# Optimization experiments

Hardware: AMD Instinct MI355X
Metric: run time of the kernel (lower is better)

## Reference

```python
import jax, jax.numpy as jnp
import numpy as np

B, X, C = 8192, 8, 512        # batch, map_num, img_dim==tex_dim
P, Y = 8, 1000                # n_prompts, cls_num
FAKE = 16                     # fake prompt width (hardcoded in module)
F = 2048                      # feat_dim
CLS = 1000                    # cls_num
IN_DIM = P * X * FAKE         # 1024
SF = 64.0


def setup_inputs() -> dict:
    key = jax.random.key(0)
    ks = jax.random.split(key, 8)
    s = 0.02
    return {
        "img_f": jax.random.normal(ks[0], (B, X, C), jnp.float32),
        "tex_f": jax.random.normal(ks[1], (P, Y, C), jnp.float32),
        "fake_cls": jax.random.normal(ks[2], (P, FAKE, C), jnp.float32),
        "fc_w": jax.random.normal(ks[3], (C, C), jnp.float32) * s,
        "fc_b": jnp.zeros((C,), jnp.float32),
        "bn1_g": jnp.ones((IN_DIM,), jnp.float32),
        "bn1_b": jnp.zeros((IN_DIM,), jnp.float32),
        "w1": jax.random.normal(ks[4], (F, IN_DIM), jnp.float32) * s,
        "b1": jnp.zeros((F,), jnp.float32),
        "bn2_g": jnp.ones((F,), jnp.float32),
        "bn2_b": jnp.zeros((F,), jnp.float32),
        "w2": jax.random.normal(ks[5], (CLS, F), jnp.float32) * s,
        "b2": jnp.zeros((CLS,), jnp.float32),
    }


def _bn(x, g, b, eps=1e-5):
    # BatchNorm1d in training mode: batch mean / biased batch var
    m = x.mean(axis=0)
    v = x.var(axis=0)
    return (x - m) * jax.lax.rsqrt(v + eps) * g + b


def reference(img_f, tex_f, fake_cls, fc_w, fc_b, bn1_g, bn1_b, w1, b1,
              bn2_g, bn2_b, w2, b2):
    # independent L2 norm over feature dim, scaled by x_sf=64
    img_n = img_f / (jnp.linalg.norm(img_f, axis=-1, keepdims=True) + 1e-6) * SF
    tex_n = tex_f / (jnp.linalg.norm(tex_f, axis=-1, keepdims=True) + 1e-6) * SF
    # prompt attention over the class axis
    tex_fc = jnp.einsum('pyc,dc->pyd', tex_n, fc_w) + fc_b          # fc(tex_f)
    attn = jax.nn.softmax(jnp.einsum('pxc,pyc->pxy', fake_cls, tex_fc), axis=-1)
    tex_a = jnp.einsum('pxy,pyc->pxc', attn, tex_n)                  # (P,16,C)
    # cross-modal relation: 'b x c, y d c -> b yxd' (icomp/tcomp are Identity)
    cp = jnp.einsum('bxc,pdc->bpxd', img_n, tex_a).reshape(img_n.shape[0], -1)
    # prt_fc: BN -> Linear -> ELU -> BN -> Linear
    h = jax.nn.elu(_bn(cp, bn1_g, bn1_b) @ w1.T + b1)
    return _bn(h, bn2_g, bn2_b) @ w2.T + b2
```

## Files before the change

### kernel.cpp

```cpp
#include <hip/hip_runtime.h>
#include <math.h>


typedef __attribute__((ext_vector_type(8))) short bf16x8;
typedef __attribute__((ext_vector_type(4))) float f32x4;

__device__ __forceinline__ float waveSum(float v) {
#pragma unroll
    for (int o = 32; o > 0; o >>= 1) v += __shfl_xor(v, o);
    return v;
}
__device__ __forceinline__ float waveMax(float v) {
#pragma unroll
    for (int o = 32; o > 0; o >>= 1) v = fmaxf(v, __shfl_xor(v, o));
    return v;
}
__device__ __forceinline__ unsigned short f2bf(float x) {
    union { float f; unsigned u; } v; v.f = x;
    unsigned r = v.u + 0x7FFFu + ((v.u >> 16) & 1u);
    return (unsigned short)(r >> 16);
}
__device__ __forceinline__ float bf2f(unsigned short h) {
    union { unsigned u; float f; } v; v.u = ((unsigned)h) << 16; return v.f;
}
__device__ __forceinline__ void gload16(const void* g, const void* l) {
    __builtin_amdgcn_global_load_lds((const __attribute__((address_space(1))) void*)g,
                                     (__attribute__((address_space(3))) void*)l, 16, 0, 0);
}
__device__ __forceinline__ int xcd_swz(int d, int n) {
    int q = n >> 3;
    return (d & 7) * q + (d >> 3);
}
#define SBAR __builtin_amdgcn_sched_barrier(0)

__global__ __launch_bounds__(256) void k_prep(const float* __restrict__ tex_f,
                                              unsigned short* __restrict__ texn,
                                              const float* __restrict__ fake_cls,
                                              const float* __restrict__ fc_w,
                                              unsigned short* __restrict__ g_bf) {
    __shared__ float sred[4];
    __shared__ float fcls[512];
    int bid = blockIdx.x, t = threadIdx.x;
    if (bid < 8000) {
        const float* r = tex_f + (size_t)bid * 512;
        float2 v = *(const float2*)(r + t * 2);
        float ss = v.x * v.x + v.y * v.y;
        ss = waveSum(ss);
        if ((t & 63) == 0) sred[t >> 6] = ss;
        __syncthreads();
        float tot = sred[0] + sred[1] + sred[2] + sred[3];
        float sc = 64.f / (sqrtf(tot) + 1e-6f);
        unsigned u = (unsigned)f2bf(v.x * sc) | ((unsigned)f2bf(v.y * sc) << 16);
        *(unsigned*)(texn + (size_t)bid * 512 + t * 2) = u;
    } else {
        int row = bid - 8000;
        fcls[t]       = fake_cls[row * 512 + t];
        fcls[t + 256] = fake_cls[row * 512 + t + 256];
        __syncthreads();
        float a0 = 0.f, a1 = 0.f;
        for (int d = 0; d < 512; ++d) {
            float fv = fcls[d];
            a0 = fmaf(fv, fc_w[d * 512 + t], a0);
            a1 = fmaf(fv, fc_w[d * 512 + t + 256], a1);
        }
        g_bf[row * 512 + t]       = f2bf(a0);
        g_bf[row * 512 + t + 256] = f2bf(a1);
    }
}

__global__ __launch_bounds__(256) void k_wsum_sm(const float* __restrict__ logit,
                                                 const unsigned short* __restrict__ texn,
                                                 float* __restrict__ part) {
    int yt = blockIdx.x, p = blockIdx.y, t = threadIdx.x;
    int lane = t & 63, w = t >> 6;
    __shared__ float wl[16][63];
    __shared__ float ms[16], iss[16];
    const int y0 = yt * 63;
    const int ylen = min(63, 1000 - y0);
#pragma unroll
    for (int rr = 0; rr < 4; ++rr) {
        int x = w * 4 + rr;
        const float* lr = logit + ((size_t)p * 16 + x) * 1000;
        float m = -3.0e38f;
        for (int y = lane; y < 1000; y += 64) m = fmaxf(m, lr[y]);
        m = waveMax(m);
        float s = 0.f;
        for (int y = lane; y < 1000; y += 64) s += expf(lr[y] - m);
        s = waveSum(s);
        if (lane == 0) { ms[x] = m; iss[x] = 1.f / s; }
    }
    __syncthreads();
    for (int idx = t; idx < 16 * ylen; idx += 256) {
        int x = idx / ylen, y = idx % ylen;
        wl[x][y] = expf(logit[((size_t)p * 16 + x) * 1000 + y0 + y] - ms[x]) * iss[x];
    }
    __syncthreads();
    int c0 = t * 2;
    const unsigned short* tp = texn + ((size_t)p * 1000 + y0) * 512 + c0;
    float a0[16], a1[16];
#pragma unroll
    for (int x = 0; x < 16; ++x) { a0[x] = 0.f; a1[x] = 0.f; }
    for (int y = 0; y < ylen; ++y) {
        unsigned u = *(const unsigned*)(tp + (size_t)y * 512);
        float lo = bf2f((unsigned short)(u & 0xffff));
        float hi = bf2f((unsigned short)(u >> 16));
#pragma unroll
        for (int x = 0; x < 16; ++x) {
            float ww = wl[x][y];
            a0[x] = fmaf(ww, lo, a0[x]);
            a1[x] = fmaf(ww, hi, a1[x]);
        }
    }
#pragma unroll
    for (int x = 0; x < 16; ++x) {
        float* dst = part + ((size_t)((yt * 8 + p) * 16 + x)) * 512 + c0;
        dst[0] = a0[x];
        dst[1] = a1[x];
    }
}

__global__ __launch_bounds__(256) void k_texa_red(const float* __restrict__ part,
                                                  unsigned short* __restrict__ texa) {
    int row = blockIdx.x, t = threadIdx.x;
    int p = row >> 4, x = row & 15;
    int c = t * 2;
    float s0 = 0.f, s1 = 0.f;
#pragma unroll
    for (int yt = 0; yt < 16; ++yt) {
        const float* src = part + ((size_t)((yt * 8 + p) * 16 + x)) * 512 + c;
        s0 += src[0];
        s1 += src[1];
    }
    unsigned u = (unsigned)f2bf(s0) | ((unsigned)f2bf(s1) << 16);
    *(unsigned*)(texa + (size_t)row * 512 + c) = u;
}

__global__ __launch_bounds__(256) void k_colstat_bf(const unsigned short* __restrict__ src,
                                                    float* __restrict__ ps,
                                                    float* __restrict__ pq, int ncols) {
    int col = blockIdx.x * 256 + threadIdx.x;
    int r0 = blockIdx.y * 128;
    const unsigned short* p = src + (size_t)r0 * ncols + col;
    float s = 0.f, q = 0.f;
    for (int r = 0; r < 128; ++r) {
        float v = bf2f(p[(size_t)r * ncols]);
        s += v;
        q = fmaf(v, v, q);
    }
    ps[(size_t)blockIdx.y * ncols + col] = s;
    pq[(size_t)blockIdx.y * ncols + col] = q;
}

template <bool PERM>
__global__ __launch_bounds__(256) void k_bnfin(const float* __restrict__ ps,
                                               const float* __restrict__ pq,
                                               const float* __restrict__ gam,
                                               const float* __restrict__ bet,
                                               float* __restrict__ a, float* __restrict__ c,
                                               int ncols) {
    int col = blockIdx.x * 256 + threadIdx.x;
    float S = 0.f, Q = 0.f;
    for (int i = 0; i < 64; ++i) {
        S += ps[(size_t)i * ncols + col];
        Q += pq[(size_t)i * ncols + col];
    }
    float mean = S * (1.f / 8192.f);
    float var = Q * (1.f / 8192.f) - mean * mean;
    int j = col;
    if (PERM) {
        int x = col >> 7, jj = col & 127, pp = jj >> 4, d = jj & 15;
        j = (pp << 7) + (x << 4) + d;
    }
    float av = gam[j] * rsqrtf(var + 1e-5f);
    a[col] = av;
    c[col] = bet[j] - mean * av;
}

template <bool PERM>
__global__ __launch_bounds__(256) void k_foldw_bf(const float* __restrict__ W,
                                                  const float* __restrict__ bin,
                                                  const float* __restrict__ a,
                                                  const float* __restrict__ c,
                                                  unsigned short* __restrict__ Wout,
                                                  float* __restrict__ bout,
                                                  int Kdim, int nvalid) {
    int f = blockIdx.x, t = threadIdx.x;
    unsigned short* wo = Wout + (size_t)f * Kdim;
    if (f >= nvalid) {
        for (int col = t; col < Kdim; col += 256) wo[col] = 0;
        if (t == 0) bout[f] = 0.f;
        return;
    }
    const float* wr = W + (size_t)f * Kdim;
    float partial = 0.f;
    for (int col = t; col < Kdim; col += 256) {
        int j = col;
        if (PERM) {
            int x = col >> 7, jj = col & 127, pp = jj >> 4, d = jj & 15;
            j = (pp << 7) + (x << 4) + d;
        }
        float wv = wr[j];
        wo[col] = f2bf(wv * a[col]);
        partial = fmaf(wv, c[col], partial);
    }
    partial = waveSum(partial);
    __shared__ float sred[4];
    if ((t & 63) == 0) sred[t >> 6] = partial;
    __syncthreads();
    if (t == 0) bout[f] = bin[f] + sred[0] + sred[1] + sred[2] + sred[3];
}

template <int EPI, bool A_F32>
__global__ __launch_bounds__(256) void gemm_mfma(const void* __restrict__ Av,
                                                 const unsigned short* __restrict__ Bv,
                                                 void* __restrict__ Cv, int K,
                                                 int ntn, int ldc, int nvalid,
                                                 int aZ, int bZ, int cZ) {
    __shared__ unsigned short Asl[128 * 64];
    __shared__ unsigned short Bsl[128 * 64];
    __shared__ float rowinv[128];
    const int tid = threadIdx.x;
    const int lane = tid & 63, wid = tid >> 6;
    const int wr = wid >> 1, wc = wid & 1;
    const int wg = xcd_swz(blockIdx.x, gridDim.x);
    const int m0 = (wg / ntn) * 128, n0 = (wg % ntn) * 128;
    const int z = blockIdx.y;

    const float* Af = (const float*)Av;
    const unsigned short* Ab = (const unsigned short*)Av + (size_t)z * aZ;
    const unsigned short* B = Bv + (size_t)z * bZ;

    f32x4 acc[4][4];
#pragma unroll
    for (int i = 0; i < 4; ++i)
#pragma unroll
        for (int j = 0; j < 4; ++j) acc[i][j] = {0.f, 0.f, 0.f, 0.f};

    const int swz = ((lane & 7) ^ (lane >> 3)) * 8;
    const int lrow = lane & 15, lkh = lane >> 4;
    float ssq[4] = {0.f, 0.f, 0.f, 0.f};

    for (int k0 = 0; k0 < K; k0 += 64) {
        if (A_F32) {
#pragma unroll
            for (int r = 0; r < 4; ++r) {
                int row = r * 32 + (tid >> 3);
                int kk = (tid & 7) * 8;
                const float* src = Af + (size_t)(m0 + row) * K + k0 + kk;
                float4 p0 = *(const float4*)src;
                float4 p1 = *(const float4*)(src + 4);
                ssq[r] += p0.x*p0.x + p0.y*p0.y + p0.z*p0.z + p0.w*p0.w
                        + p1.x*p1.x + p1.y*p1.y + p1.z*p1.z + p1.w*p1.w;
                bf16x8 v;
                v[0] = (short)f2bf(p0.x); v[1] = (short)f2bf(p0.y);
                v[2] = (short)f2bf(p0.z); v[3] = (short)f2bf(p0.w);
                v[4] = (short)f2bf(p1.x); v[5] = (short)f2bf(p1.y);
                v[6] = (short)f2bf(p1.z); v[7] = (short)f2bf(p1.w);
                *(bf16x8*)&Asl[row * 64 + (kk ^ ((row & 7) << 3))] = v;
            }
        } else {
#pragma unroll
            for (int r = 0; r < 4; ++r) {
                int row = r * 32 + wid * 8 + (lane >> 3);
                gload16(Ab + (size_t)(m0 + row) * K + k0 + swz,
                        Asl + r * 2048 + wid * 512);
            }
        }
#pragma unroll
        for (int r = 0; r < 4; ++r) {
            int row = r * 32 + wid * 8 + (lane >> 3);
            gload16(B + (size_t)(n0 + row) * K + k0 + swz,
                    Bsl + r * 2048 + wid * 512);
        }
        __syncthreads();
#pragma unroll
        for (int kk = 0; kk < 2; ++kk) {
            bf16x8 af[4], bfr[4];
#pragma unroll
            for (int m = 0; m < 4; ++m) {
                int row = wr * 64 + m * 16 + lrow;
                af[m] = *(const bf16x8*)&Asl[row * 64 + ((kk * 32 + lkh * 8) ^ ((row & 7) << 3))];
            }
#pragma unroll
            for (int n = 0; n < 4; ++n) {
                int row = wc * 64 + n * 16 + lrow;
                bfr[n] = *(const bf16x8*)&Bsl[row * 64 + ((kk * 32 + lkh * 8) ^ ((row & 7) << 3))];
            }
#pragma unroll
            for (int m = 0; m < 4; ++m)
#pragma unroll
                for (int n = 0; n < 4; ++n)
                    acc[m][n] = __builtin_amdgcn_mfma_f32_16x16x32_bf16(af[m], bfr[n], acc[m][n], 0, 0, 0);
        }
        __syncthreads();
    }

    if (A_F32) {
#pragma unroll
        for (int r = 0; r < 4; ++r) {
            float s = ssq[r];
            s += __shfl_xor(s, 1); s += __shfl_xor(s, 2); s += __shfl_xor(s, 4);
            if ((tid & 7) == 0) rowinv[r * 32 + (tid >> 3)] = 64.f / (sqrtf(s) + 1e-6f);
        }
        __syncthreads();
    }

    const int colbase = n0 + wc * 64 + lrow;
    if (EPI == 0) {
        unsigned short* C = (unsigned short*)Cv;
#pragma unroll
        for (int m = 0; m < 4; ++m) {
            int rloc = wr * 64 + m * 16 + lkh * 4;
#pragma unroll
            for (int r = 0; r < 4; ++r) {
                float riv = rowinv[rloc + r];
#pragma unroll
                for (int n = 0; n < 4; ++n)
                    C[(size_t)(m0 + rloc + r) * ldc + colbase + n * 16] = f2bf(acc[m][n][r] * riv);
            }
        }
    } else {
        float* C = (float*)Cv + (size_t)z * cZ;
#pragma unroll
        for (int m = 0; m < 4; ++m) {
            int row = m0 + wr * 64 + m * 16 + lkh * 4;
#pragma unroll
            for (int r = 0; r < 4; ++r) {
                if ((row + r) >= 16) continue;
#pragma unroll
                for (int n = 0; n < 4; ++n) {
                    int col = colbase + n * 16;
                    if (col < nvalid) C[(size_t)(row + r) * ldc + col] = acc[m][n][r];
                }
            }
        }
    }
}

template <int FM, int NH, int EPI>
__global__ __launch_bounds__(512, 2) void gemm256(const unsigned short* __restrict__ A,
                                                  const unsigned short* __restrict__ B,
                                                  void* __restrict__ Cv, int K,
                                                  int ntn, int ldc, int nvalid,
                                                  const float* __restrict__ bias,
                                                  float* __restrict__ ps,
                                                  float* __restrict__ pq) {
    constexpr int BM = FM * 32;
    constexpr int MH = BM / 128;
    constexpr int BN = NH * 128;
    constexpr int LA = 2 * (MH + NH);
    __shared__ unsigned short Asl[2][MH][128 * 64];
    __shared__ unsigned short Bsl[2][NH][128 * 64];
    const int tid = threadIdx.x;
    const int lane = tid & 63, wid = tid >> 6;
    const int wm = wid >> 2, wn = wid & 3;
    const int wg = xcd_swz(blockIdx.x, gridDim.x);
    const int m0 = (wg / ntn) * BM, n0 = (wg % ntn) * BN;
    const int lrow = lane & 15, lkh = lane >> 4;
    const int l7 = lane & 7;
    const int ksrc = ((lane & 7) ^ (lane >> 3)) * 8;
    const int mbase = wm * (BM / 2);
    const int mhalf = mbase >> 7;
    const int mloc0 = mbase & 127;
    const int nbase = wn * 64;
    const int nhalf = nbase >> 7;
    const int nloc0 = nbase & 127;

    f32x4 acc[FM][4];
#pragma unroll
    for (int m = 0; m < FM; ++m)
#pragma unroll
        for (int n = 0; n < 4; ++n) acc[m][n] = {0.f, 0.f, 0.f, 0.f};

    const int nkt = K >> 6;

    auto stage = [&](int kt, int buf) {
#pragma unroll
        for (int hf = 0; hf < MH; ++hf)
#pragma unroll
            for (int j = 0; j < 2; ++j) {
                int rl = wid * 16 + j * 8 + (lane >> 3);
                gload16(A + (size_t)(m0 + hf * 128 + rl) * K + kt * 64 + ksrc,
                        &Asl[buf][hf][(wid * 16 + j * 8) * 64]);
            }
#pragma unroll
        for (int hf = 0; hf < NH; ++hf)
#pragma unroll
            for (int j = 0; j < 2; ++j) {
                int rl = wid * 16 + j * 8 + (lane >> 3);
                gload16(B + (size_t)(n0 + hf * 128 + rl) * K + kt * 64 + ksrc,
                        &Bsl[buf][hf][(wid * 16 + j * 8) * 64]);
            }
    };

    stage(0, 0);
    stage(1, 1);
    if constexpr (LA == 8) asm volatile("s_waitcnt vmcnt(8)" ::: "memory");
    else asm volatile("s_waitcnt vmcnt(6)" ::: "memory");
    SBAR; __builtin_amdgcn_s_barrier(); SBAR;

    for (int kt = 0; kt < nkt; ++kt) {
        const int cur = kt & 1;
        bf16x8 af0[FM], bf0[4];
#pragma unroll
        for (int m = 0; m < FM; ++m) {
            int row = mloc0 + m * 16 + lrow;
            af0[m] = *(const bf16x8*)&Asl[cur][mhalf][row * 64 + ((lkh ^ l7) << 3)];
        }
#pragma unroll
        for (int n = 0; n < 4; ++n) {
            int row = nloc0 + n * 16 + lrow;
            bf0[n] = *(const bf16x8*)&Bsl[cur][nhalf][row * 64 + ((lkh ^ l7) << 3)];
        }
        __builtin_amdgcn_s_setprio(1);
#pragma unroll
        for (int m = 0; m < FM; ++m)
#pragma unroll
            for (int n = 0; n < 4; ++n)
                acc[m][n] = __builtin_amdgcn_mfma_f32_16x16x32_bf16(af0[m], bf0[n], acc[m][n], 0, 0, 0);
        __builtin_amdgcn_s_setprio(0);
        bf16x8 af1[FM], bf1[4];
#pragma unroll
        for (int m = 0; m < FM; ++m) {
            int row = mloc0 + m * 16 + lrow;
            af1[m] = *(const bf16x8*)&Asl[cur][mhalf][row * 64 + (((4 + lkh) ^ l7) << 3)];
        }
#pragma unroll
        for (int n = 0; n < 4; ++n) {
            int row = nloc0 + n * 16 + lrow;
            bf1[n] = *(const bf16x8*)&Bsl[cur][nhalf][row * 64 + (((4 + lkh) ^ l7) << 3)];
        }
        if (kt + 1 < nkt) {
            asm volatile("s_waitcnt lgkmcnt(0)" ::: "memory");
            SBAR; __builtin_amdgcn_s_barrier(); SBAR;
            if (kt + 2 < nkt) {
                stage(kt + 2, cur);
                if constexpr (LA == 8) asm volatile("s_waitcnt vmcnt(8)" ::: "memory");
                else asm volatile("s_waitcnt vmcnt(6)" ::: "memory");
            } else {
                asm volatile("s_waitcnt vmcnt(0)" ::: "memory");
            }
            SBAR; __builtin_amdgcn_s_barrier(); SBAR;
        }
        __builtin_amdgcn_s_setprio(1);
#pragma unroll
        for (int m = 0; m < FM; ++m)
#pragma unroll
            for (int n = 0; n < 4; ++n)
                acc[m][n] = __builtin_amdgcn_mfma_f32_16x16x32_bf16(af1[m], bf1[n], acc[m][n], 0, 0, 0);
        __builtin_amdgcn_s_setprio(0);
    }

    const int colbase = n0 + nbase + lrow;
    if (EPI == 1) {
        unsigned short* C = (unsigned short*)Cv;
        float bv[4], sN[4] = {0.f, 0.f, 0.f, 0.f}, qN[4] = {0.f, 0.f, 0.f, 0.f};
#pragma unroll
        for (int n = 0; n < 4; ++n) bv[n] = bias[colbase + n * 16];
#pragma unroll
        for (int m = 0; m < FM; ++m) {
            int row = m0 + mbase + m * 16 + lkh * 4;
#pragma unroll
            for (int r = 0; r < 4; ++r)
#pragma unroll
                for (int n = 0; n < 4; ++n) {
                    float v = acc[m][n][r] + bv[n];
                    v = v > 0.f ? v : expm1f(v);
                    sN[n] += v;
                    qN[n] = fmaf(v, v, qN[n]);
                    C[(size_t)(row + r) * ldc + colbase + n * 16] = f2bf(v);
                }
        }
#pragma unroll
        for (int n = 0; n < 4; ++n) {
            sN[n] += __shfl_xor(sN[n], 16); sN[n] += __shfl_xor(sN[n], 32);
            qN[n] += __shfl_xor(qN[n], 16); qN[n] += __shfl_xor(qN[n], 32);
        }
        if (lane < 16) {
            int mt = wg / ntn;
#pragma unroll
            for (int n = 0; n < 4; ++n) {
                ps[(size_t)(mt * 2 + wm) * ldc + colbase + n * 16] = sN[n];
                pq[(size_t)(mt * 2 + wm) * ldc + colbase + n * 16] = qN[n];
            }
        }
    } else {
        float* C = (float*)Cv;
        float bv[4];
#pragma unroll
        for (int n = 0; n < 4; ++n) bv[n] = bias[colbase + n * 16];
#pragma unroll
        for (int m = 0; m < FM; ++m) {
            int row = m0 + mbase + m * 16 + lkh * 4;
#pragma unroll
            for (int r = 0; r < 4; ++r)
#pragma unroll
                for (int n = 0; n < 4; ++n) {
                    int col = colbase + n * 16;
                    if (col < nvalid) C[(size_t)(row + r) * ldc + col] = acc[m][n][r] + bv[n];
                }
        }
    }
}

extern "C" void kernel_launch(void* const* d_in, const int* in_sizes, int n_in,
                              void* d_out, int out_size, void* d_ws, size_t ws_size,
                              hipStream_t stream) {
    const float* img_f    = (const float*)d_in[0];
    const float* tex_f    = (const float*)d_in[1];
    const float* fake_cls = (const float*)d_in[2];
    const float* fc_w     = (const float*)d_in[3];
    const float* bn1_g    = (const float*)d_in[5];
    const float* bn1_b    = (const float*)d_in[6];
    const float* w1       = (const float*)d_in[7];
    const float* b1       = (const float*)d_in[8];
    const float* bn2_g    = (const float*)d_in[9];
    const float* bn2_b    = (const float*)d_in[10];
    const float* w2       = (const float*)d_in[11];
    const float* b2       = (const float*)d_in[12];
    float* out = (float*)d_out;

    char* w = (char*)d_ws;
    unsigned short* texn = (unsigned short*)(w);
    unsigned short* g_bf = (unsigned short*)(w + 8388608);
    float*          logit= (float*)(w + 8650752);
    float*          part = (float*)(w + 9175040);
    unsigned short* texa = (unsigned short*)(w + 13369344);
    unsigned short* cp   = (unsigned short*)(w + 13500416);
    unsigned short* w1a  = (unsigned short*)(w + 30277632);
    float*          b1p  = (float*)(w + 34471936);
    float*          a1   = (float*)(w + 34480128);
    float*          c1   = (float*)(w + 34484224);
    float*          ps   = (float*)(w + 34488320);
    float*          pq   = (float*)(w + 35012608);
    unsigned short* h    = (unsigned short*)(w + 35536896);
    unsigned short* w2a  = (unsigned short*)(w + 69091328);
    float*          b2p  = (float*)(w + 73285632);
    float*          a2   = (float*)(w + 73289728);
    float*          c2   = (float*)(w + 73297920);

    k_prep<<<8128, 256, 0, stream>>>(tex_f, texn, fake_cls, fc_w, g_bf);
    gemm_mfma<3, false><<<dim3(8, 8), 256, 0, stream>>>(
        g_bf, texn, logit, 512, 8, 1000, 1000, 16 * 512, 1000 * 512, 16 * 1000);
    k_wsum_sm<<<dim3(16, 8), 256, 0, stream>>>(logit, texn, part);
    k_texa_red<<<128, 256, 0, stream>>>(part, texa);

    gemm_mfma<0, true><<<dim3(512, 1), 256, 0, stream>>>(
        img_f, texa, cp, 512, 1, 128, 128, 0, 0, 0);

    k_colstat_bf<<<dim3(4, 64), 256, 0, stream>>>(cp, ps, pq, 1024);
    k_bnfin<true><<<4, 256, 0, stream>>>(ps, pq, bn1_g, bn1_b, a1, c1, 1024);
    k_foldw_bf<true><<<2048, 256, 0, stream>>>(w1, b1, a1, c1, w1a, b1p, 1024, 2048);

    gemm256<8, 2, 1><<<dim3(256), 512, 0, stream>>>(
        cp, w1a, h, 1024, 8, 2048, 2048, b1p, ps, pq);

    k_bnfin<false><<<8, 256, 0, stream>>>(ps, pq, bn2_g, bn2_b, a2, c2, 2048);
    k_foldw_bf<false><<<1024, 256, 0, stream>>>(w2, b2, a2, c2, w2a, b2p, 2048, 1000);

    gemm256<4, 2, 2><<<dim3(256), 512, 0, stream>>>(
        h, w2a, out, 2048, 4, 1000, 1000, b2p, nullptr, nullptr);
}
```

Baseline: 240.8 us.

## Fuse small reduction kernels via atomics and last-block, restructure gemm256 pipeline

The texa partial-sum reduction kernel is replaced by float atomicAdd into a zeroed f32 buffer, and the fp32 texa is converted to bf16 inside the cp GEMM's B loader. Both BN finalize kernels are folded into the preceding stat-producing kernels using a last-block-done counter pattern. The gemm256 main loop is reorganized to interleave global prefetch loads with MFMA phases. Together these cut kernel launches and overlap loads with compute, at the cost of a memset, atomics, and a serial last-block finalize.

Measured after the change: 400.5 us. 66.3% more time.

```diff
diff --git a/kernel.cpp b/kernel.cpp
--- a/kernel.cpp
+++ b/kernel.cpp
@@ -70,7 +70,7 @@
 
 __global__ __launch_bounds__(256) void k_wsum_sm(const float* __restrict__ logit,
                                                  const unsigned short* __restrict__ texn,
-                                                 float* __restrict__ part) {
+                                                 float* __restrict__ texa_f32) {
     int yt = blockIdx.x, p = blockIdx.y, t = threadIdx.x;
     int lane = t & 63, w = t >> 6;
     __shared__ float wl[16][63];
@@ -113,31 +113,21 @@
     }
 #pragma unroll
     for (int x = 0; x < 16; ++x) {
-        float* dst = part + ((size_t)((yt * 8 + p) * 16 + x)) * 512 + c0;
-        dst[0] = a0[x];
-        dst[1] = a1[x];
-    }
-}
-
-__global__ __launch_bounds__(256) void k_texa_red(const float* __restrict__ part,
-                                                  unsigned short* __restrict__ texa) {
-    int row = blockIdx.x, t = threadIdx.x;
-    int p = row >> 4, x = row & 15;
-    int c = t * 2;
-    float s0 = 0.f, s1 = 0.f;
-#pragma unroll
-    for (int yt = 0; yt < 16; ++yt) {
-        const float* src = part + ((size_t)((yt * 8 + p) * 16 + x)) * 512 + c;
-        s0 += src[0];
-        s1 += src[1];
-    }
-    unsigned u = (unsigned)f2bf(s0) | ((unsigned)f2bf(s1) << 16);
-    *(unsigned*)(texa + (size_t)row * 512 + c) = u;
-}
-
-__global__ __launch_bounds__(256) void k_colstat_bf(const unsigned short* __restrict__ src,
-                                                    float* __restrict__ ps,
-                                                    float* __restrict__ pq, int ncols) {
+        float* dst = texa_f32 + (size_t)(p * 16 + x) * 512 + c0;
+        atomicAdd(dst, a0[x]);
+        atomicAdd(dst + 1, a1[x]);
+    }
+}
+
+__global__ __launch_bounds__(256) void k_colstat_bn1(const unsigned short* __restrict__ src,
+                                                     float* __restrict__ ps,
+                                                     float* __restrict__ pq,
+                                                     const float* __restrict__ gam,
+                                                     const float* __restrict__ bet,
+                                                     float* __restrict__ a1,
+                                                     float* __restrict__ c1,
+                                                     unsigned* __restrict__ cnt) {
+    const int ncols = 1024;
     int col = blockIdx.x * 256 + threadIdx.x;
     int r0 = blockIdx.y * 128;
     const unsigned short* p = src + (size_t)r0 * ncols + col;
@@ -149,31 +139,29 @@
     }
     ps[(size_t)blockIdx.y * ncols + col] = s;
     pq[(size_t)blockIdx.y * ncols + col] = q;
-}
-
-template <bool PERM>
-__global__ __launch_bounds__(256) void k_bnfin(const float* __restrict__ ps,
-                                               const float* __restrict__ pq,
-                                               const float* __restrict__ gam,
-                                               const float* __restrict__ bet,
-                                               float* __restrict__ a, float* __restrict__ c,
-                                               int ncols) {
-    int col = blockIdx.x * 256 + threadIdx.x;
-    float S = 0.f, Q = 0.f;
-    for (int i = 0; i < 64; ++i) {
-        S += ps[(size_t)i * ncols + col];
-        Q += pq[(size_t)i * ncols + col];
-    }
-    float mean = S * (1.f / 8192.f);
-    float var = Q * (1.f / 8192.f) - mean * mean;
-    int j = col;
-    if (PERM) {
-        int x = col >> 7, jj = col & 127, pp = jj >> 4, d = jj & 15;
-        j = (pp << 7) + (x << 4) + d;
-    }
-    float av = gam[j] * rsqrtf(var + 1e-5f);
-    a[col] = av;
-    c[col] = bet[j] - mean * av;
+    __shared__ bool amLast;
+    __threadfence();
+    __syncthreads();
+    if (threadIdx.x == 0)
+        amLast = (atomicAdd(cnt, 1u) == gridDim.x * gridDim.y - 1);
+    __syncthreads();
+    if (amLast) {
+        __threadfence();
+        for (int c = threadIdx.x; c < 1024; c += 256) {
+            float S = 0.f, Q = 0.f;
+            for (int i = 0; i < 64; ++i) {
+                S += ps[(size_t)i * ncols + c];
+                Q += pq[(size_t)i * ncols + c];
+            }
+            float mean = S * (1.f / 8192.f);
+            float var = Q * (1.f / 8192.f) - mean * mean;
+            int x = c >> 7, jj = c & 127, pp = jj >> 4, d = jj & 15;
+            int j = (pp << 7) + (x << 4) + d;
+            float av = gam[j] * rsqrtf(var + 1e-5f);
+            a1[c] = av;
+            c1[c] = bet[j] - mean * av;
+        }
+    }
 }
 
 template <bool PERM>
@@ -212,7 +200,7 @@
 
 template <int EPI, bool A_F32>
 __global__ __launch_bounds__(256) void gemm_mfma(const void* __restrict__ Av,
-                                                 const unsigned short* __restrict__ Bv,
+                                                 const void* __restrict__ Bv,
                                                  void* __restrict__ Cv, int K,
                                                  int ntn, int ldc, int nvalid,
                                                  int aZ, int bZ, int cZ) {
@@ -227,8 +215,9 @@
     const int z = blockIdx.y;
 
     const float* Af = (const float*)Av;
+    const float* Bf = (const float*)Bv;
     const unsigned short* Ab = (const unsigned short*)Av + (size_t)z * aZ;
-    const unsigned short* B = Bv + (size_t)z * bZ;
+    const unsigned short* Bb = (const unsigned short*)Bv + (size_t)z * bZ;
 
     f32x4 acc[4][4];
 #pragma unroll
@@ -258,6 +247,20 @@
                 v[6] = (short)f2bf(p1.z); v[7] = (short)f2bf(p1.w);
                 *(bf16x8*)&Asl[row * 64 + (kk ^ ((row & 7) << 3))] = v;
             }
+#pragma unroll
+            for (int r = 0; r < 4; ++r) {
+                int row = r * 32 + (tid >> 3);
+                int kk = (tid & 7) * 8;
+                const float* src = Bf + (size_t)(n0 + row) * K + k0 + kk;
+                float4 p0 = *(const float4*)src;
+                float4 p1 = *(const float4*)(src + 4);
+                bf16x8 v;
+                v[0] = (short)f2bf(p0.x); v[1] = (short)f2bf(p0.y);
+                v[2] = (short)f2bf(p0.z); v[3] = (short)f2bf(p0.w);
+                v[4] = (short)f2bf(p1.x); v[5] = (short)f2bf(p1.y);
+                v[6] = (short)f2bf(p1.z); v[7] = (short)f2bf(p1.w);
+                *(bf16x8*)&Bsl[row * 64 + (kk ^ ((row & 7) << 3))] = v;
+            }
         } else {
 #pragma unroll
             for (int r = 0; r < 4; ++r) {
@@ -265,12 +268,12 @@
                 gload16(Ab + (size_t)(m0 + row) * K + k0 + swz,
                         Asl + r * 2048 + wid * 512);
             }
-        }
-#pragma unroll
-        for (int r = 0; r < 4; ++r) {
-            int row = r * 32 + wid * 8 + (lane >> 3);
-            gload16(B + (size_t)(n0 + row) * K + k0 + swz,
-                    Bsl + r * 2048 + wid * 512);
+#pragma unroll
+            for (int r = 0; r < 4; ++r) {
+                int row = r * 32 + wid * 8 + (lane >> 3);
+                gload16(Bb + (size_t)(n0 + row) * K + k0 + swz,
+                        Bsl + r * 2048 + wid * 512);
+            }
         }
         __syncthreads();
 #pragma unroll
@@ -344,22 +347,27 @@
                                                   int ntn, int ldc, int nvalid,
                                                   const float* __restrict__ bias,
                                                   float* __restrict__ ps,
-                                                  float* __restrict__ pq) {
-    constexpr int BM = FM * 32;
-    constexpr int MH = BM / 128;
-    constexpr int BN = NH * 128;
-    constexpr int LA = 2 * (MH + NH);
+                                                  float* __restrict__ pq,
+                                                  const float* __restrict__ gam,
+                                                  const float* __restrict__ bet,
+                                                  float* __restrict__ aout,
+                                                  float* __restrict__ cout,
+                                                  unsigned* __restrict__ cnt) {
+    constexpr int MH = (FM * 32) / 128;
+    constexpr int LA = 2 * MH + 2 * NH;
+    constexpr int NPH = (FM == 8) ? 4 : 2;
+    constexpr int LPP = LA / NPH;
     __shared__ unsigned short Asl[2][MH][128 * 64];
     __shared__ unsigned short Bsl[2][NH][128 * 64];
     const int tid = threadIdx.x;
     const int lane = tid & 63, wid = tid >> 6;
     const int wm = wid >> 2, wn = wid & 3;
     const int wg = xcd_swz(blockIdx.x, gridDim.x);
-    const int m0 = (wg / ntn) * BM, n0 = (wg % ntn) * BN;
+    const int m0 = (wg / ntn) * (FM * 32), n0 = (wg % ntn) * 256;
     const int lrow = lane & 15, lkh = lane >> 4;
     const int l7 = lane & 7;
     const int ksrc = ((lane & 7) ^ (lane >> 3)) * 8;
-    const int mbase = wm * (BM / 2);
+    const int mbase = wm * (FM * 16);
     const int mhalf = mbase >> 7;
     const int mloc0 = mbase & 127;
     const int nbase = wn * 64;
@@ -374,81 +382,77 @@
 
     const int nkt = K >> 6;
 
-    auto stage = [&](int kt, int buf) {
-#pragma unroll
-        for (int hf = 0; hf < MH; ++hf)
-#pragma unroll
-            for (int j = 0; j < 2; ++j) {
-                int rl = wid * 16 + j * 8 + (lane >> 3);
-                gload16(A + (size_t)(m0 + hf * 128 + rl) * K + kt * 64 + ksrc,
-                        &Asl[buf][hf][(wid * 16 + j * 8) * 64]);
-            }
-#pragma unroll
-        for (int hf = 0; hf < NH; ++hf)
-#pragma unroll
-            for (int j = 0; j < 2; ++j) {
-                int rl = wid * 16 + j * 8 + (lane >> 3);
-                gload16(B + (size_t)(n0 + hf * 128 + rl) * K + kt * 64 + ksrc,
-                        &Bsl[buf][hf][(wid * 16 + j * 8) * 64]);
-            }
+    auto stage1 = [&](int kt, int buf, int idx) {
+        int rl = wid * 16 + (idx & 1) * 8 + (lane >> 3);
+        int dst = (wid * 16 + (idx & 1) * 8) * 64;
+        if (idx < 2 * MH) {
+            gload16(A + (size_t)(m0 + (idx >> 1) * 128 + rl) * K + kt * 64 + ksrc,
+                    &Asl[buf][idx >> 1][dst]);
+        } else {
+            int ii = idx - 2 * MH;
+            gload16(B + (size_t)(n0 + (ii >> 1) * 128 + rl) * K + kt * 64 + ksrc,
+                    &Bsl[buf][ii >> 1][dst]);
+        }
     };
 
-    stage(0, 0);
-    stage(1, 1);
-    if constexpr (LA == 8) asm volatile("s_waitcnt vmcnt(8)" ::: "memory");
-    else asm volatile("s_waitcnt vmcnt(6)" ::: "memory");
+#pragma unroll
+    for (int l = 0; l < LA; ++l) stage1(0, 0, l);
+#pragma unroll
+    for (int l = 0; l < LA; ++l) stage1(1, 1, l);
+    asm volatile("s_waitcnt vmcnt(%0)" :: "i"(LA) : "memory");
     SBAR; __builtin_amdgcn_s_barrier(); SBAR;
 
     for (int kt = 0; kt < nkt; ++kt) {
         const int cur = kt & 1;
-        bf16x8 af0[FM], bf0[4];
-#pragma unroll
-        for (int m = 0; m < FM; ++m) {
-            int row = mloc0 + m * 16 + lrow;
-            af0[m] = *(const bf16x8*)&Asl[cur][mhalf][row * 64 + ((lkh ^ l7) << 3)];
-        }
-#pragma unroll
-        for (int n = 0; n < 4; ++n) {
-            int row = nloc0 + n * 16 + lrow;
-            bf0[n] = *(const bf16x8*)&Bsl[cur][nhalf][row * 64 + ((lkh ^ l7) << 3)];
-        }
-        __builtin_amdgcn_s_setprio(1);
-#pragma unroll
-        for (int m = 0; m < FM; ++m)
-#pragma unroll
-            for (int n = 0; n < 4; ++n)
-                acc[m][n] = __builtin_amdgcn_mfma_f32_16x16x32_bf16(af0[m], bf0[n], acc[m][n], 0, 0, 0);
-        __builtin_amdgcn_s_setprio(0);
-        bf16x8 af1[FM], bf1[4];
-#pragma unroll
-        for (int m = 0; m < FM; ++m) {
-            int row = mloc0 + m * 16 + lrow;
-            af1[m] = *(const bf16x8*)&Asl[cur][mhalf][row * 64 + (((4 + lkh) ^ l7) << 3)];
-        }
-#pragma unroll
-        for (int n = 0; n < 4; ++n) {
-            int row = nloc0 + n * 16 + lrow;
-            bf1[n] = *(const bf16x8*)&Bsl[cur][nhalf][row * 64 + (((4 + lkh) ^ l7) << 3)];
-        }
-        if (kt + 1 < nkt) {
+        bf16x8 afr[2][FM], bfr[2][4];
+#pragma unroll
+        for (int h = 0; h < 2; ++h) {
+#pragma unroll
+            for (int m = 0; m < FM; ++m) {
+                int row = mloc0 + m * 16 + lrow;
+                afr[h][m] = *(const bf16x8*)&Asl[cur][mhalf][row * 64 + (((h * 4 + lkh) ^ l7) << 3)];
+            }
+#pragma unroll
+            for (int n = 0; n < 4; ++n) {
+                int row = nloc0 + n * 16 + lrow;
+                bfr[h][n] = *(const bf16x8*)&Bsl[cur][nhalf][row * 64 + (((h * 4 + lkh) ^ l7) << 3)];
+            }
+        }
+        const bool notlast = (kt + 1 < nkt);
+        const bool pf = (kt + 2 < nkt);
+        if (notlast) {
             asm volatile("s_waitcnt lgkmcnt(0)" ::: "memory");
-            SBAR; __builtin_amdgcn_s_barrier(); SBAR;
-            if (kt + 2 < nkt) {
-                stage(kt + 2, cur);
-                if constexpr (LA == 8) asm volatile("s_waitcnt vmcnt(8)" ::: "memory");
-                else asm volatile("s_waitcnt vmcnt(6)" ::: "memory");
-            } else {
-                asm volatile("s_waitcnt vmcnt(0)" ::: "memory");
-            }
-            SBAR; __builtin_amdgcn_s_barrier(); SBAR;
-        }
-        __builtin_amdgcn_s_setprio(1);
-#pragma unroll
-        for (int m = 0; m < FM; ++m)
-#pragma unroll
-            for (int n = 0; n < 4; ++n)
-                acc[m][n] = __builtin_amdgcn_mfma_f32_16x16x32_bf16(af1[m], bf1[n], acc[m][n], 0, 0, 0);
-        __builtin_amdgcn_s_setprio(0);
+            SBAR;
+            __builtin_amdgcn_s_barrier();
+            SBAR;
+        }
+#pragma unroll
+        for (int q = 0; q < NPH; ++q) {
+            if (pf) {
+#pragma unroll
+                for (int l = 0; l < LPP; ++l) stage1(kt + 2, cur, q * LPP + l);
+                SBAR;
+            }
+            __builtin_amdgcn_s_setprio(1);
+            constexpr int MG = FM / ((NPH == 4) ? 2 : 1);
+            const int h = (NPH == 4) ? (q >> 1) : q;
+            const int g0 = (NPH == 4) ? (q & 1) * MG : 0;
+#pragma unroll
+            for (int mm = 0; mm < MG; ++mm)
+#pragma unroll
+                for (int n = 0; n < 4; ++n)
+                    acc[g0 + mm][n] = __builtin_amdgcn_mfma_f32_16x16x32_bf16(
+                        afr[h][g0 + mm], bfr[h][n], acc[g0 + mm][n], 0, 0, 0);
+            __builtin_amdgcn_s_setprio(0);
+            SBAR;
+        }
+        if (notlast) {
+            if (pf) asm volatile("s_waitcnt vmcnt(%0)" :: "i"(LA) : "memory");
+            else    asm volatile("s_waitcnt vmcnt(0)" ::: "memory");
+            SBAR;
+            __builtin_amdgcn_s_barrier();
+            SBAR;
+        }
     }
 
     const int colbase = n0 + nbase + lrow;
@@ -482,6 +486,26 @@
             for (int n = 0; n < 4; ++n) {
                 ps[(size_t)(mt * 2 + wm) * ldc + colbase + n * 16] = sN[n];
                 pq[(size_t)(mt * 2 + wm) * ldc + colbase + n * 16] = qN[n];
+            }
+        }
+        __shared__ bool amLast;
+        __threadfence();
+        __syncthreads();
+        if (tid == 0) amLast = (atomicAdd(cnt, 1u) == gridDim.x - 1);
+        __syncthreads();
+        if (amLast) {
+            __threadfence();
+            for (int c = tid; c < 2048; c += 512) {
+                float S = 0.f, Q = 0.f;
+                for (int i = 0; i < 64; ++i) {
+                    S += ps[(size_t)i * 2048 + c];
+                    Q += pq[(size_t)i * 2048 + c];
+                }
+                float mean = S * (1.f / 8192.f);
+                float var = Q * (1.f / 8192.f) - mean * mean;
+                float av = gam[c] * rsqrtf(var + 1e-5f);
+                aout[c] = av;
+                cout[c] = bet[c] - mean * av;
             }
         }
     } else {
@@ -521,43 +545,43 @@
     float* out = (float*)d_out;
 
     char* w = (char*)d_ws;
-    unsigned short* texn = (unsigned short*)(w);
-    unsigned short* g_bf = (unsigned short*)(w + 8388608);
-    float*          logit= (float*)(w + 8650752);
-    float*          part = (float*)(w + 9175040);
-    unsigned short* texa = (unsigned short*)(w + 13369344);
-    unsigned short* cp   = (unsigned short*)(w + 13500416);
-    unsigned short* w1a  = (unsigned short*)(w + 30277632);
-    float*          b1p  = (float*)(w + 34471936);
-    float*          a1   = (float*)(w + 34480128);
-    float*          c1   = (float*)(w + 34484224);
-    float*          ps   = (float*)(w + 34488320);
-    float*          pq   = (float*)(w + 35012608);
-    unsigned short* h    = (unsigned short*)(w + 35536896);
-    unsigned short* w2a  = (unsigned short*)(w + 69091328);
-    float*          b2p  = (float*)(w + 73285632);
-    float*          a2   = (float*)(w + 73289728);
-    float*          c2   = (float*)(w + 73297920);
+    unsigned*       cnt  = (unsigned*)(w);
+    float*          texaf= (float*)(w + 256);
+    unsigned short* texn = (unsigned short*)(w + 270336);
+    unsigned short* g_bf = (unsigned short*)(w + 8658944);
+    float*          logit= (float*)(w + 8921088);
+    unsigned short* cp   = (unsigned short*)(w + 9445376);
+    unsigned short* w1a  = (unsigned short*)(w + 26222592);
+    float*          b1p  = (float*)(w + 30416896);
+    float*          a1   = (float*)(w + 30425088);
+    float*          c1   = (float*)(w + 30429184);
+    float*          ps   = (float*)(w + 30433280);
+    float*          pq   = (float*)(w + 30957568);
+    unsigned short* h    = (unsigned short*)(w + 31481856);
+    unsigned short* w2a  = (unsigned short*)(w + 65036288);
+    float*          b2p  = (float*)(w + 69230592);
+    float*          a2   = (float*)(w + 69234688);
+    float*          c2   = (float*)(w + 69242880);
+
+    hipMemsetAsync(w, 0, 262400, stream);
 
     k_prep<<<8128, 256, 0, stream>>>(tex_f, texn, fake_cls, fc_w, g_bf);
     gemm_mfma<3, false><<<dim3(8, 8), 256, 0, stream>>>(
         g_bf, texn, logit, 512, 8, 1000, 1000, 16 * 512, 1000 * 512, 16 * 1000);
-    k_wsum_sm<<<dim3(16, 8), 256, 0, stream>>>(logit, texn, part);
-    k_texa_red<<<128, 256, 0, stream>>>(part, texa);
+    k_wsum_sm<<<dim3(16, 8), 256, 0, stream>>>(logit, texn, texaf);
 
     gemm_mfma<0, true><<<dim3(512, 1), 256, 0, stream>>>(
-        img_f, texa, cp, 512, 1, 128, 128, 0, 0, 0);
-
-    k_colstat_bf<<<dim3(4, 64), 256, 0, stream>>>(cp, ps, pq, 1024);
-    k_bnfin<true><<<4, 256, 0, stream>>>(ps, pq, bn1_g, bn1_b, a1, c1, 1024);
+        img_f, texaf, cp, 512, 1, 128, 128, 0, 0, 0);
+
+    k_colstat_bn1<<<dim3(4, 64), 256, 0, stream>>>(cp, ps, pq, bn1_g, bn1_b, a1, c1, cnt + 1);
     k_foldw_bf<true><<<2048, 256, 0, stream>>>(w1, b1, a1, c1, w1a, b1p, 1024, 2048);
 
     gemm256<8, 2, 1><<<dim3(256), 512, 0, stream>>>(
-        cp, w1a, h, 1024, 8, 2048, 2048, b1p, ps, pq);
-
-    k_bnfin<false><<<8, 256, 0, stream>>>(ps, pq, bn2_g, bn2_b, a2, c2, 2048);
+        cp, w1a, h, 1024, 8, 2048, 2048, b1p, ps, pq, bn2_g, bn2_b, a2, c2, cnt);
+
     k_foldw_bf<false><<<1024, 256, 0, stream>>>(w2, b2, a2, c2, w2a, b2p, 2048, 1000);
 
     gemm256<4, 2, 2><<<dim3(256), 512, 0, stream>>>(
-        h, w2a, out, 2048, 4, 1000, 1000, b2p, nullptr, nullptr);
-}
+        h, w2a, out, 2048, 4, 1000, 1000, b2p, nullptr, nullptr,
+        nullptr, nullptr, nullptr, nullptr, nullptr);
+}
```
